# Optimization experiments

Measured on AMD Instinct MI355X. Metric: run time of the kernel, lower is better.

## Reference

```python
import jax, jax.numpy as jnp
import numpy as np

B, IN, HID, OUT, E, C, TOPK = 4096, 1024, 2048, 1024, 8, 1000, 2
EPS = 1e-6


def setup_inputs() -> dict:
    key = jax.random.key(0)
    ks = jax.random.split(key, 8)
    def xavier(k, fan_out, fan_in):
        lim = float(np.sqrt(6.0 / (fan_in + fan_out)))
        return jax.random.uniform(k, (fan_out, fan_in), jnp.float32, -lim, lim)
    return {
        "x": jax.random.normal(ks[0], (B, IN), jnp.float32),
        "Wg": xavier(ks[1], E, IN),
        "bg": jnp.zeros((E,), jnp.float32),
        "gamma": jnp.ones((1, E), jnp.float32),
        "beta": jnp.zeros((1, E), jnp.float32),
        "W1": xavier(ks[2], HID * E, IN),
        "b1": jnp.zeros((HID * E,), jnp.float32),
        "W2": xavier(ks[3], OUT * E, HID * E),
        "b2": jnp.zeros((OUT * E,), jnp.float32),
        "Wc": xavier(ks[4], C, OUT),
        "bc": jnp.zeros((C,), jnp.float32),
    }


def reference(x, Wg, bg, gamma, beta, W1, b1, W2, b2, Wc, bc):
    # gating (noise_std=0 -> no noise)
    gate_logits = x @ Wg.T + bg                      # [B, E]
    # GRN over expert dim
    Gx = jnp.linalg.norm(gate_logits, axis=1, keepdims=True)   # [B, 1]
    Nx = Gx / (jnp.mean(Gx, axis=0, keepdims=True) + EPS)      # [B, 1]
    gate_logits = gamma * (gate_logits * Nx) + beta
    gate_probs = jax.nn.softmax(gate_logits, axis=-1)
    topk_probs, topk_idx = jax.lax.top_k(gate_probs, TOPK)     # [B, K]
    # dense all-expert MLP (fc2 mixes across ALL experts' hidden units, as in source)
    h = jax.nn.relu(x @ W1.T + b1)                   # [B, HID*E]
    eo = (h @ W2.T + b2).reshape(B, E, OUT)          # [B, E, OUT]
    sel = jnp.take_along_axis(eo, topk_idx[:, :, None], axis=1)  # [B, K, OUT]
    out = jnp.einsum('bk,bkd->bd', topk_probs, sel)  # [B, OUT]
    return out @ Wc.T + bc                           # [B, C]
```

## Files before the change

kernel.cpp:

```cpp
#include <hip/hip_runtime.h>
#include <stdint.h>

#define B_SZ   4096
#define IN_SZ  1024
#define NE     8
#define NC     1000
#define HIDE   16384
#define OUTE   1024
#define GEPS   1e-6f

typedef __attribute__((ext_vector_type(8))) short short8;
typedef __attribute__((ext_vector_type(4))) float floatx4;

__device__ __forceinline__ unsigned short f2bf(float f) {
    unsigned u = __float_as_uint(f);
    u += 0x7fffu + ((u >> 16) & 1u);
    return (unsigned short)(u >> 16);
}
__device__ __forceinline__ float bf2f(unsigned short h) {
    return __uint_as_float(((unsigned)h) << 16);
}

__device__ __forceinline__ void async16(const void* g, void* l) {
    __builtin_amdgcn_global_load_lds(
        (const __attribute__((address_space(1))) void*)g,
        (__attribute__((address_space(3))) void*)l, 16, 0, 0);
}

__global__ __launch_bounds__(256) void k_cvt(const float* __restrict__ src,
                                             unsigned short* __restrict__ dst, int n) {
    int i = (blockIdx.x * 256 + threadIdx.x) * 4;
    int stride = gridDim.x * 256 * 4;
    for (; i < n; i += stride) {
        float4 v = *(const float4*)(src + i);
        ushort4 o;
        o.x = f2bf(v.x); o.y = f2bf(v.y); o.z = f2bf(v.z); o.w = f2bf(v.w);
        *(ushort4*)(dst + i) = o;
    }
}

__global__ __launch_bounds__(256) void k_gate(const float* __restrict__ x,
                                              const float* __restrict__ Wg,
                                              const float* __restrict__ bg,
                                              float* __restrict__ logits,
                                              float* __restrict__ Gx) {
    int wid = threadIdx.x >> 6, lane = threadIdx.x & 63;
    int b = blockIdx.x * 4 + wid;
    const float* xr = x + (size_t)b * IN_SZ;
    float xv[16];
#pragma unroll
    for (int t = 0; t < 16; ++t) xv[t] = xr[lane + 64 * t];
    float lg[NE];
#pragma unroll
    for (int e = 0; e < NE; ++e) {
        const float* wr = Wg + e * IN_SZ;
        float s = 0.f;
#pragma unroll
        for (int t = 0; t < 16; ++t) s += xv[t] * wr[lane + 64 * t];
#pragma unroll
        for (int m = 32; m >= 1; m >>= 1) s += __shfl_xor(s, m, 64);
        lg[e] = s + bg[e];
    }
    if (lane == 0) {
        float ss = 0.f;
#pragma unroll
        for (int e = 0; e < NE; ++e) { logits[b * NE + e] = lg[e]; ss += lg[e] * lg[e]; }
        Gx[b] = sqrtf(ss);
    }
}

__global__ __launch_bounds__(1024) void k_gsum(const float* __restrict__ Gx, float* __restrict__ gsum) {
    __shared__ float sm[1024];
    int t = threadIdx.x;
    sm[t] = Gx[t] + Gx[t + 1024] + Gx[t + 2048] + Gx[t + 3072];
    __syncthreads();
    for (int m = 512; m >= 1; m >>= 1) {
        if (t < m) sm[t] += sm[t + m];
        __syncthreads();
    }
    if (t == 0) gsum[0] = sm[0];
}

__global__ void k_zeroctrl(int* ctrl) {
    if (threadIdx.x < 24) ctrl[threadIdx.x] = 0;
}

__global__ __launch_bounds__(256) void k_topk(const float* __restrict__ logits,
                                              const float* __restrict__ Gx,
                                              const float* __restrict__ gsum,
                                              const float* __restrict__ gamma,
                                              const float* __restrict__ beta,
                                              int* __restrict__ tidx, float* __restrict__ tp,
                                              int* __restrict__ counts) {
    int b = blockIdx.x * 256 + threadIdx.x;
    float nx = Gx[b] / (gsum[0] * (1.0f / (float)B_SZ) + GEPS);
    float l[NE];
    float mx = -1e30f;
#pragma unroll
    for (int e = 0; e < NE; ++e) {
        l[e] = gamma[e] * (logits[b * NE + e] * nx) + beta[e];
        mx = fmaxf(mx, l[e]);
    }
    float se = 0.f;
#pragma unroll
    for (int e = 0; e < NE; ++e) { l[e] = expf(l[e] - mx); se += l[e]; }
    float inv = 1.f / se;
    int i0 = 0; float p0 = l[0];
#pragma unroll
    for (int e = 1; e < NE; ++e) if (l[e] > p0) { p0 = l[e]; i0 = e; }
    int i1 = -1; float p1 = -1.f;
#pragma unroll
    for (int e = 0; e < NE; ++e) if (e != i0 && l[e] > p1) { p1 = l[e]; i1 = e; }
    tidx[b * 2 + 0] = i0; tidx[b * 2 + 1] = i1;
    tp[b * 2 + 0] = p0 * inv; tp[b * 2 + 1] = p1 * inv;
    atomicAdd(&counts[i0], 1);
    atomicAdd(&counts[i1], 1);
}

__global__ void k_offsets(const int* __restrict__ counts, int* __restrict__ offs) {
    if (threadIdx.x == 0) {
        int a = 0;
        for (int e = 0; e < NE; ++e) { offs[e] = a; a += counts[e]; }
    }
}

__global__ __launch_bounds__(256) void k_fill(const int* __restrict__ tidx, const float* __restrict__ tp,
                                              const int* __restrict__ offs, int* __restrict__ cursors,
                                              int* __restrict__ rowsw, float* __restrict__ probsw) {
    int b = blockIdx.x * 256 + threadIdx.x;
#pragma unroll
    for (int k = 0; k < 2; ++k) {
        int e = tidx[b * 2 + k];
        int pos = atomicAdd(&cursors[e], 1);
        int at = offs[e] + pos;
        rowsw[at] = b * 2 + k;
        probsw[at] = tp[b * 2 + k];
    }
}

__device__ __forceinline__ void gemm_core(const unsigned short* sa0, const unsigned short* sa1,
                                          const unsigned short* sb0, const unsigned short* sb1,
                                          short* sA, short* sB, int nkt, int wid, int lane,
                                          floatx4 acc[4][4]) {
    short* ldsA0 = sA + (wid * 2 + 0) * 512;
    short* ldsA1 = sA + (wid * 2 + 1) * 512;
    short* ldsB0 = sB + (wid * 2 + 0) * 512;
    short* ldsB1 = sB + (wid * 2 + 1) * 512;
    const int wm = wid >> 1, wn = wid & 1;
    int aoff[4], boff[4];
#pragma unroll
    for (int i = 0; i < 4; ++i) {
        aoff[i] = (wm * 64 + i * 16 + (lane & 15)) * 32 + (lane >> 4) * 8;
        boff[i] = (wn * 64 + i * 16 + (lane & 15)) * 32 + (lane >> 4) * 8;
    }
    for (int kt = 0; kt < nkt; ++kt) {
        __syncthreads();
        async16(sa0, ldsA0);
        async16(sa1, ldsA1);
        async16(sb0, ldsB0);
        async16(sb1, ldsB1);
        sa0 += 32; sa1 += 32; sb0 += 32; sb1 += 32;
        __syncthreads();
        short8 av[4], bv[4];
#pragma unroll
        for (int i = 0; i < 4; ++i) av[i] = *(const short8*)(sA + aoff[i]);
#pragma unroll
        for (int j = 0; j < 4; ++j) bv[j] = *(const short8*)(sB + boff[j]);
#pragma unroll
        for (int i = 0; i < 4; ++i)
#pragma unroll
            for (int j = 0; j < 4; ++j)
                acc[i][j] = __builtin_amdgcn_mfma_f32_16x16x32_bf16(av[i], bv[j], acc[i][j], 0, 0, 0);
    }
}

__global__ __launch_bounds__(256) void k_gemm_h(const unsigned short* __restrict__ xb,
                                                const unsigned short* __restrict__ w1b,
                                                const float* __restrict__ b1,
                                                unsigned short* __restrict__ h) {
    __shared__ __align__(16) short sA[128 * 32];
    __shared__ __align__(16) short sB[128 * 32];
    const int lane = threadIdx.x & 63, wid = threadIdx.x >> 6;
    const int mt = blockIdx.x & 31, nt = blockIdx.x >> 5;
    const int m0 = mt * 128, n0 = nt * 128;
    const int t0row = (wid * 2 + 0) * 16 + (lane >> 2);
    const int t1row = (wid * 2 + 1) * 16 + (lane >> 2);
    const int kb = (lane & 3) * 8;
    const unsigned short* sa0 = xb + (size_t)(m0 + t0row) * IN_SZ + kb;
    const unsigned short* sa1 = xb + (size_t)(m0 + t1row) * IN_SZ + kb;
    const unsigned short* sb0 = w1b + (size_t)(n0 + t0row) * IN_SZ + kb;
    const unsigned short* sb1 = w1b + (size_t)(n0 + t1row) * IN_SZ + kb;
    floatx4 acc[4][4] = {};
    gemm_core(sa0, sa1, sb0, sb1, sA, sB, IN_SZ / 32, wid, lane, acc);
    const int wm = wid >> 1, wn = wid & 1;
#pragma unroll
    for (int i = 0; i < 4; ++i)
#pragma unroll
        for (int j = 0; j < 4; ++j)
#pragma unroll
            for (int r = 0; r < 4; ++r) {
                int row = m0 + wm * 64 + i * 16 + (lane >> 4) * 4 + r;
                int col = n0 + wn * 64 + j * 16 + (lane & 15);
                float v = acc[i][j][r] + b1[col];
                h[(size_t)row * HIDE + col] = f2bf(fmaxf(v, 0.f));
            }
}

__global__ __launch_bounds__(256) void k_gemm_moe(const unsigned short* __restrict__ h,
                                                  const unsigned short* __restrict__ w2b,
                                                  const float* __restrict__ b2,
                                                  const int* __restrict__ counts,
                                                  const int* __restrict__ offs,
                                                  const int* __restrict__ rowsw,
                                                  const float* __restrict__ probsw,
                                                  unsigned short* __restrict__ slotbuf) {
    const int bid = blockIdx.x;
    const int e = bid >> 8;
    const int rem = bid & 255;
    const int mt = rem >> 3, nt = rem & 7;
    const int gn = counts[e];
    if (mt * 128 >= gn) return;
    const int gbase = offs[e];
    __shared__ __align__(16) short sA[128 * 32];
    __shared__ __align__(16) short sB[128 * 32];
    const int lane = threadIdx.x & 63, wid = threadIdx.x >> 6;
    const int t0row = (wid * 2 + 0) * 16 + (lane >> 2);
    const int t1row = (wid * 2 + 1) * 16 + (lane >> 2);
    const int kb = (lane & 3) * 8;
    int g0 = mt * 128 + t0row; if (g0 > gn - 1) g0 = gn - 1;
    int g1 = mt * 128 + t1row; if (g1 > gn - 1) g1 = gn - 1;
    const int rv0 = rowsw[gbase + g0] >> 1;
    const int rv1 = rowsw[gbase + g1] >> 1;
    const int n0 = nt * 128;
    const unsigned short* sa0 = h + (size_t)rv0 * HIDE + kb;
    const unsigned short* sa1 = h + (size_t)rv1 * HIDE + kb;
    const unsigned short* sb0 = w2b + (size_t)(e * OUTE + n0 + t0row) * HIDE + kb;
    const unsigned short* sb1 = w2b + (size_t)(e * OUTE + n0 + t1row) * HIDE + kb;
    floatx4 acc[4][4] = {};
    gemm_core(sa0, sa1, sb0, sb1, sA, sB, HIDE / 32, wid, lane, acc);
    const int wm = wid >> 1, wn = wid & 1;
#pragma unroll
    for (int i = 0; i < 4; ++i)
#pragma unroll
        for (int j = 0; j < 4; ++j)
#pragma unroll
            for (int r = 0; r < 4; ++r) {
                int lr = mt * 128 + wm * 64 + i * 16 + (lane >> 4) * 4 + r;
                if (lr < gn) {
                    int at = gbase + lr;
                    int dest = rowsw[at];
                    float p = probsw[at];
                    int col = n0 + wn * 64 + j * 16 + (lane & 15);
                    float v = (acc[i][j][r] + b2[e * OUTE + col]) * p;
                    slotbuf[(size_t)dest * OUTE + col] = f2bf(v);
                }
            }
}

__global__ __launch_bounds__(256) void k_combine(const unsigned short* __restrict__ slotbuf,
                                                 unsigned short* __restrict__ ymix) {
    int i = blockIdx.x * 256 + threadIdx.x;
    int b = i >> 7;
    int d = (i & 127) * 8;
    short8 s0 = *(const short8*)(slotbuf + (size_t)(b * 2 + 0) * OUTE + d);
    short8 s1 = *(const short8*)(slotbuf + (size_t)(b * 2 + 1) * OUTE + d);
    short8 o;
#pragma unroll
    for (int t = 0; t < 8; ++t)
        o[t] = (short)f2bf(bf2f((unsigned short)s0[t]) + bf2f((unsigned short)s1[t]));
    *(short8*)(ymix + (size_t)b * OUTE + d) = o;
}

__global__ __launch_bounds__(256) void k_gemm_out(const unsigned short* __restrict__ ymix,
                                                  const unsigned short* __restrict__ wcb,
                                                  const float* __restrict__ bc,
                                                  float* __restrict__ out) {
    const int mt = blockIdx.x >> 3, nt = blockIdx.x & 7;
    const int m0 = mt * 128, n0 = nt * 128;
    __shared__ __align__(16) short sA[128 * 32];
    __shared__ __align__(16) short sB[128 * 32];
    const int lane = threadIdx.x & 63, wid = threadIdx.x >> 6;
    const int t0row = (wid * 2 + 0) * 16 + (lane >> 2);
    const int t1row = (wid * 2 + 1) * 16 + (lane >> 2);
    const int kb = (lane & 3) * 8;
    int br0 = n0 + t0row; if (br0 > NC - 1) br0 = NC - 1;
    int br1 = n0 + t1row; if (br1 > NC - 1) br1 = NC - 1;
    const unsigned short* sa0 = ymix + (size_t)(m0 + t0row) * IN_SZ + kb;
    const unsigned short* sa1 = ymix + (size_t)(m0 + t1row) * IN_SZ + kb;
    const unsigned short* sb0 = wcb + (size_t)br0 * IN_SZ + kb;
    const unsigned short* sb1 = wcb + (size_t)br1 * IN_SZ + kb;
    floatx4 acc[4][4] = {};
    gemm_core(sa0, sa1, sb0, sb1, sA, sB, IN_SZ / 32, wid, lane, acc);
    const int wm = wid >> 1, wn = wid & 1;
#pragma unroll
    for (int i = 0; i < 4; ++i)
#pragma unroll
        for (int j = 0; j < 4; ++j)
#pragma unroll
            for (int r = 0; r < 4; ++r) {
                int row = m0 + wm * 64 + i * 16 + (lane >> 4) * 4 + r;
                int col = n0 + wn * 64 + j * 16 + (lane & 15);
                if (col < NC)
                    out[(size_t)row * NC + col] = acc[i][j][r] + bc[col];
            }
}

extern "C" void kernel_launch(void* const* d_in, const int* in_sizes, int n_in,
                              void* d_out, int out_size, void* d_ws, size_t ws_size,
                              hipStream_t stream) {
    const float* x     = (const float*)d_in[0];
    const float* Wg    = (const float*)d_in[1];
    const float* bg    = (const float*)d_in[2];
    const float* gamma = (const float*)d_in[3];
    const float* beta  = (const float*)d_in[4];
    const float* W1    = (const float*)d_in[5];
    const float* b1    = (const float*)d_in[6];
    const float* W2    = (const float*)d_in[7];
    const float* b2    = (const float*)d_in[8];
    const float* Wc    = (const float*)d_in[9];
    const float* bc    = (const float*)d_in[10];
    float* out = (float*)d_out;

    char* ws = (char*)d_ws;
    size_t o = 0;
    auto carve = [&](size_t bytes) { char* p = ws + o; o += (bytes + 255) & ~(size_t)255; return p; };
    unsigned short* xb   = (unsigned short*)carve((size_t)B_SZ * IN_SZ * 2);
    unsigned short* w1b  = (unsigned short*)carve((size_t)HIDE * IN_SZ * 2);
    unsigned short* w2b  = (unsigned short*)carve((size_t)NE * OUTE * HIDE * 2);
    unsigned short* wcb  = (unsigned short*)carve((size_t)NC * IN_SZ * 2);
    unsigned short* h    = (unsigned short*)carve((size_t)B_SZ * HIDE * 2);
    unsigned short* slot = (unsigned short*)carve((size_t)B_SZ * 2 * OUTE * 2);
    unsigned short* ymix = (unsigned short*)carve((size_t)B_SZ * OUTE * 2);
    float* logits = (float*)carve((size_t)B_SZ * NE * 4);
    float* Gx     = (float*)carve((size_t)B_SZ * 4);
    int*   tidx   = (int*)carve((size_t)B_SZ * 2 * 4);
    float* tp     = (float*)carve((size_t)B_SZ * 2 * 4);
    int*   rowsw  = (int*)carve((size_t)B_SZ * 2 * 4);
    float* probsw = (float*)carve((size_t)B_SZ * 2 * 4);
    int*   ctrl   = (int*)carve(256);
    int* counts  = ctrl;
    int* cursors = ctrl + 8;
    int* offs    = ctrl + 16;
    float* gsum  = (float*)(ctrl + 24);

    k_cvt<<<2048, 256, 0, stream>>>(x,  xb,  B_SZ * IN_SZ);
    k_cvt<<<2048, 256, 0, stream>>>(W1, w1b, HIDE * IN_SZ);
    k_cvt<<<2048, 256, 0, stream>>>(W2, w2b, NE * OUTE * HIDE);
    k_cvt<<<2048, 256, 0, stream>>>(Wc, wcb, NC * IN_SZ);

    k_gate<<<B_SZ / 4, 256, 0, stream>>>(x, Wg, bg, logits, Gx);
    k_gsum<<<1, 1024, 0, stream>>>(Gx, gsum);
    k_zeroctrl<<<1, 64, 0, stream>>>(ctrl);
    k_topk<<<B_SZ / 256, 256, 0, stream>>>(logits, Gx, gsum, gamma, beta, tidx, tp, counts);
    k_offsets<<<1, 64, 0, stream>>>(counts, offs);
    k_fill<<<B_SZ / 256, 256, 0, stream>>>(tidx, tp, offs, cursors, rowsw, probsw);

    k_gemm_h<<<32 * (HIDE / 128), 256, 0, stream>>>(xb, w1b, b1, h);
    k_gemm_moe<<<NE * 32 * 8, 256, 0, stream>>>(h, w2b, b2, counts, offs, rowsw, probsw, slot);
    k_combine<<<(B_SZ * OUTE / 8) / 256, 256, 0, stream>>>(slot, ymix);
    k_gemm_out<<<32 * 8, 256, 0, stream>>>(ymix, wcb, bc, out);
}
```

Before: 1.018 ms.

## Replace both big GEMMs with 256x256 double-buffered 8-wave kernels and split-K MoE

The fc1 and per-expert fc2 GEMMs move from 128x128 single-buffered tiles to 256x256 tiles with 512 threads and 128KB of dynamic LDS. The new kernels use XOR-swizzled LDS layouts, double buffering with staged async loads, setprio around MFMA groups, and an XCD-aware block remap. The MoE GEMM is split four ways along K into bf16 partial buffers. A new reduce kernel sums the partials, adds bias and applies the gate-weighted combine, replacing the old epilogue and combine kernel. This aims to raise MFMA utilisation and data reuse, at the cost of extra partial-buffer traffic and bf16 rounding of the partial sums.

Measured after the change: 1.274 ms. 1.25x slower.

```diff
diff --git a/kernel.cpp b/kernel.cpp
--- a/kernel.cpp
+++ b/kernel.cpp
@@ -8,6 +8,10 @@
 #define HIDE   16384
 #define OUTE   1024
 #define GEPS   1e-6f
+#define NSPLIT 4
+#define KSPL   4096
+#define NT_MOE 64
+#define NT_H   16
 
 typedef __attribute__((ext_vector_type(8))) short short8;
 typedef __attribute__((ext_vector_type(4))) float floatx4;
@@ -25,6 +29,12 @@
     __builtin_amdgcn_global_load_lds(
         (const __attribute__((address_space(1))) void*)g,
         (__attribute__((address_space(3))) void*)l, 16, 0, 0);
+}
+
+__device__ __forceinline__ void stage_half(const unsigned short* p0, const unsigned short* p1,
+                                           char* smemc, int ldsoff, int w, int tt) {
+    async16(p0 + (size_t)tt * 64, smemc + ldsoff + w * 1024);
+    async16(p1 + (size_t)tt * 64, smemc + ldsoff + 8192 + w * 1024);
 }
 
 __global__ __launch_bounds__(256) void k_cvt(const float* __restrict__ src,
@@ -126,7 +136,7 @@
 
 __global__ __launch_bounds__(256) void k_fill(const int* __restrict__ tidx, const float* __restrict__ tp,
                                               const int* __restrict__ offs, int* __restrict__ cursors,
-                                              int* __restrict__ rowsw, float* __restrict__ probsw) {
+                                              int* __restrict__ rowsw, int* __restrict__ slotof) {
     int b = blockIdx.x * 256 + threadIdx.x;
 #pragma unroll
     for (int k = 0; k < 2; ++k) {
@@ -134,8 +144,196 @@
         int pos = atomicAdd(&cursors[e], 1);
         int at = offs[e] + pos;
         rowsw[at] = b * 2 + k;
-        probsw[at] = tp[b * 2 + k];
-    }
+        slotof[b * 2 + k] = at;
+    }
+}
+
+
+#define MFMA_PAIR(JA, JB) \
+  __builtin_amdgcn_s_setprio(1); \
+  _Pragma("unroll") \
+  for (int i_ = 0; i_ < 8; ++i_) { \
+    acc[i_][JA] = __builtin_amdgcn_mfma_f32_16x16x32_bf16(av[i_], bva, acc[i_][JA], 0, 0, 0); \
+    acc[i_][JB] = __builtin_amdgcn_mfma_f32_16x16x32_bf16(av[i_], bvb, acc[i_][JB], 0, 0, 0); \
+  } \
+  __builtin_amdgcn_s_setprio(0);
+
+#define BARSYNC  __builtin_amdgcn_s_barrier(); __builtin_amdgcn_sched_barrier(0);
+
+#define TILE_BODY(T_, BUF_, NTT_) do { \
+  const int tq1_ = (T_) + 1, tq2_ = (T_) + 2; \
+  if (tq1_ < (NTT_)) { \
+    stage_half(pA[1][0], pA[1][1], smemc, ((tq1_ & 1) * 65536) + 16384, w, tq1_); \
+    asm volatile("s_waitcnt vmcnt(4)" ::: "memory"); \
+  } else { \
+    asm volatile("s_waitcnt vmcnt(0)" ::: "memory"); \
+  } \
+  BARSYNC \
+  { \
+  const short* Ab_ = smem + (BUF_) * 32768 + wm * 8192; \
+  const short* Bb_ = smem + (BUF_) * 32768 + 16384 + (wn >> 1) * 8192; \
+  short8 av[8], bva, bvb; \
+  _Pragma("unroll") \
+  for (int i_ = 0; i_ < 8; ++i_) av[i_] = *(const short8*)(Ab_ + aoff[i_]); \
+  bva = *(const short8*)(Bb_ + boff[0]); \
+  bvb = *(const short8*)(Bb_ + boff[1]); \
+  MFMA_PAIR(0, 1) \
+  BARSYNC \
+  bva = *(const short8*)(Bb_ + boff[2]); \
+  bvb = *(const short8*)(Bb_ + boff[3]); \
+  if (tq1_ < (NTT_)) stage_half(pB[0][0], pB[0][1], smemc, ((tq1_ & 1) * 65536) + 32768, w, tq1_); \
+  MFMA_PAIR(2, 3) \
+  BARSYNC \
+  _Pragma("unroll") \
+  for (int i_ = 0; i_ < 8; ++i_) av[i_] = *(const short8*)(Ab_ + (aoff[i_] ^ 32)); \
+  bva = *(const short8*)(Bb_ + (boff[0] ^ 32)); \
+  bvb = *(const short8*)(Bb_ + (boff[1] ^ 32)); \
+  if (tq1_ < (NTT_)) stage_half(pB[1][0], pB[1][1], smemc, ((tq1_ & 1) * 65536) + 49152, w, tq1_); \
+  MFMA_PAIR(0, 1) \
+  BARSYNC \
+  bva = *(const short8*)(Bb_ + (boff[2] ^ 32)); \
+  bvb = *(const short8*)(Bb_ + (boff[3] ^ 32)); \
+  if (tq2_ < (NTT_)) stage_half(pA[0][0], pA[0][1], smemc, ((tq2_ & 1) * 65536) + 0, w, tq2_); \
+  MFMA_PAIR(2, 3) \
+  BARSYNC \
+  } \
+} while (0)
+
+#define CORE_PROLOGUE(NTT_) \
+  stage_half(pA[0][0], pA[0][1], smemc, 0,     w, 0); \
+  stage_half(pA[1][0], pA[1][1], smemc, 16384, w, 0); \
+  stage_half(pB[0][0], pB[0][1], smemc, 32768, w, 0); \
+  stage_half(pB[1][0], pB[1][1], smemc, 49152, w, 0); \
+  if ((NTT_) > 1) stage_half(pA[0][0], pA[0][1], smemc, 65536, w, 1);
+
+__global__ __launch_bounds__(512, 1) void k_h8(const unsigned short* __restrict__ xb,
+                                               const unsigned short* __restrict__ w1b,
+                                               const float* __restrict__ b1,
+                                               unsigned short* __restrict__ hout) {
+    extern __shared__ short smem[];
+    char* smemc = (char*)smem;
+    const int tid = threadIdx.x, lane = tid & 63, w = tid >> 6;
+    const int wm = w >> 2, wn = w & 3;
+    const int q = gridDim.x >> 3;
+    const int wg = (blockIdx.x & 7) * q + (blockIdx.x >> 3);
+    const int mt = wg & 15, nt = wg >> 4;
+    const int m0 = mt * 256, n0 = nt * 256;
+    const int ccs = ((lane & 7) ^ (lane >> 3)) * 8;
+    const unsigned short* pA[2][2];
+    const unsigned short* pB[2][2];
+#pragma unroll
+    for (int h = 0; h < 2; ++h)
+#pragma unroll
+        for (int c = 0; c < 2; ++c) {
+            pA[h][c] = xb  + (size_t)(m0 + h * 128 + c * 64 + w * 8 + (lane >> 3)) * IN_SZ + ccs;
+            pB[h][c] = w1b + (size_t)(n0 + h * 128 + c * 64 + w * 8 + (lane >> 3)) * IN_SZ + ccs;
+        }
+    int aoff[8], boff[4];
+#pragma unroll
+    for (int i = 0; i < 8; ++i)
+        aoff[i] = (i * 16 + (lane & 15)) * 64 + (((lane >> 4) ^ (lane & 7)) * 8);
+#pragma unroll
+    for (int j = 0; j < 4; ++j)
+        boff[j] = ((wn & 1) * 64 + j * 16 + (lane & 15)) * 64 + (((lane >> 4) ^ (lane & 7)) * 8);
+    floatx4 acc[8][4] = {};
+    CORE_PROLOGUE(NT_H)
+    for (int t = 0; t < NT_H; t += 2) { TILE_BODY(t, 0, NT_H); TILE_BODY(t + 1, 1, NT_H); }
+#pragma unroll
+    for (int i = 0; i < 8; ++i)
+#pragma unroll
+        for (int j = 0; j < 4; ++j)
+#pragma unroll
+            for (int r = 0; r < 4; ++r) {
+                int row = m0 + wm * 128 + i * 16 + (lane >> 4) * 4 + r;
+                int col = n0 + wn * 64 + j * 16 + (lane & 15);
+                float v = acc[i][j][r] + b1[col];
+                hout[(size_t)row * HIDE + col] = f2bf(fmaxf(v, 0.f));
+            }
+}
+
+__global__ __launch_bounds__(512, 1) void k_moe8(const unsigned short* __restrict__ h,
+                                                 const unsigned short* __restrict__ w2b,
+                                                 const int* __restrict__ counts,
+                                                 const int* __restrict__ offs,
+                                                 const int* __restrict__ rowsw,
+                                                 unsigned short* __restrict__ parts) {
+    extern __shared__ short smem[];
+    char* smemc = (char*)smem;
+    const int q = gridDim.x >> 3;
+    const int wg = (blockIdx.x & 7) * q + (blockIdx.x >> 3);
+    const int mt = wg & 15, sp = (wg >> 4) & 3, nt = (wg >> 6) & 3, e = wg >> 8;
+    const int gn = counts[e];
+    if (mt * 256 >= gn) return;
+    const int gbase = offs[e];
+    const int tid = threadIdx.x, lane = tid & 63, w = tid >> 6;
+    const int wm = w >> 2, wn = w & 3;
+    const int ccs = ((lane & 7) ^ (lane >> 3)) * 8;
+    const unsigned short* pA[2][2];
+    const unsigned short* pB[2][2];
+#pragma unroll
+    for (int hh = 0; hh < 2; ++hh)
+#pragma unroll
+        for (int c = 0; c < 2; ++c) {
+            int lr = mt * 256 + hh * 128 + c * 64 + w * 8 + (lane >> 3);
+            if (lr > gn - 1) lr = gn - 1;
+            int grow = rowsw[gbase + lr] >> 1;
+            pA[hh][c] = h + (size_t)grow * HIDE + sp * KSPL + ccs;
+            int brow = e * OUTE + nt * 256 + hh * 128 + c * 64 + w * 8 + (lane >> 3);
+            pB[hh][c] = w2b + (size_t)brow * HIDE + sp * KSPL + ccs;
+        }
+    int aoff[8], boff[4];
+#pragma unroll
+    for (int i = 0; i < 8; ++i)
+        aoff[i] = (i * 16 + (lane & 15)) * 64 + (((lane >> 4) ^ (lane & 7)) * 8);
+#pragma unroll
+    for (int j = 0; j < 4; ++j)
+        boff[j] = ((wn & 1) * 64 + j * 16 + (lane & 15)) * 64 + (((lane >> 4) ^ (lane & 7)) * 8);
+    floatx4 acc[8][4] = {};
+    CORE_PROLOGUE(NT_MOE)
+    for (int t = 0; t < NT_MOE; t += 2) { TILE_BODY(t, 0, NT_MOE); TILE_BODY(t + 1, 1, NT_MOE); }
+    unsigned short* pbase = parts + (size_t)sp * B_SZ * 2 * OUTE;
+#pragma unroll
+    for (int i = 0; i < 8; ++i)
+#pragma unroll
+        for (int j = 0; j < 4; ++j)
+#pragma unroll
+            for (int r = 0; r < 4; ++r) {
+                int lr = mt * 256 + wm * 128 + i * 16 + (lane >> 4) * 4 + r;
+                if (lr < gn) {
+                    int at = gbase + lr;
+                    int col = nt * 256 + wn * 64 + j * 16 + (lane & 15);
+                    pbase[(size_t)at * OUTE + col] = f2bf(acc[i][j][r]);
+                }
+            }
+}
+
+__global__ __launch_bounds__(256) void k_reduce(const unsigned short* __restrict__ parts,
+                                                const int* __restrict__ slotof,
+                                                const int* __restrict__ tidx,
+                                                const float* __restrict__ tp,
+                                                const float* __restrict__ b2,
+                                                unsigned short* __restrict__ ymix) {
+    int i = blockIdx.x * 256 + threadIdx.x;
+    int b = i >> 8, col = (i & 255) * 4;
+    int at0 = slotof[b * 2], at1 = slotof[b * 2 + 1];
+    int e0 = tidx[b * 2], e1 = tidx[b * 2 + 1];
+    float q0 = tp[b * 2], q1 = tp[b * 2 + 1];
+    float y0[4] = {0.f, 0.f, 0.f, 0.f}, y1[4] = {0.f, 0.f, 0.f, 0.f};
+#pragma unroll
+    for (int sp = 0; sp < NSPLIT; ++sp) {
+        ushort4 u0 = *(const ushort4*)(parts + ((size_t)sp * B_SZ * 2 + at0) * OUTE + col);
+        ushort4 u1 = *(const ushort4*)(parts + ((size_t)sp * B_SZ * 2 + at1) * OUTE + col);
+        y0[0] += bf2f(u0.x); y0[1] += bf2f(u0.y); y0[2] += bf2f(u0.z); y0[3] += bf2f(u0.w);
+        y1[0] += bf2f(u1.x); y1[1] += bf2f(u1.y); y1[2] += bf2f(u1.z); y1[3] += bf2f(u1.w);
+    }
+    float4 bb0 = *(const float4*)(b2 + (size_t)e0 * OUTE + col);
+    float4 bb1 = *(const float4*)(b2 + (size_t)e1 * OUTE + col);
+    ushort4 o;
+    o.x = f2bf(q0 * (y0[0] + bb0.x) + q1 * (y1[0] + bb1.x));
+    o.y = f2bf(q0 * (y0[1] + bb0.y) + q1 * (y1[1] + bb1.y));
+    o.z = f2bf(q0 * (y0[2] + bb0.z) + q1 * (y1[2] + bb1.z));
+    o.w = f2bf(q0 * (y0[3] + bb0.w) + q1 * (y1[3] + bb1.w));
+    *(ushort4*)(ymix + (size_t)b * OUTE + col) = o;
 }
 
 __device__ __forceinline__ void gemm_core(const unsigned short* sa0, const unsigned short* sa1,
@@ -172,103 +370,6 @@
             for (int j = 0; j < 4; ++j)
                 acc[i][j] = __builtin_amdgcn_mfma_f32_16x16x32_bf16(av[i], bv[j], acc[i][j], 0, 0, 0);
     }
-}
-
-__global__ __launch_bounds__(256) void k_gemm_h(const unsigned short* __restrict__ xb,
-                                                const unsigned short* __restrict__ w1b,
-                                                const float* __restrict__ b1,
-                                                unsigned short* __restrict__ h) {
-    __shared__ __align__(16) short sA[128 * 32];
-    __shared__ __align__(16) short sB[128 * 32];
-    const int lane = threadIdx.x & 63, wid = threadIdx.x >> 6;
-    const int mt = blockIdx.x & 31, nt = blockIdx.x >> 5;
-    const int m0 = mt * 128, n0 = nt * 128;
-    const int t0row = (wid * 2 + 0) * 16 + (lane >> 2);
-    const int t1row = (wid * 2 + 1) * 16 + (lane >> 2);
-    const int kb = (lane & 3) * 8;
-    const unsigned short* sa0 = xb + (size_t)(m0 + t0row) * IN_SZ + kb;
-    const unsigned short* sa1 = xb + (size_t)(m0 + t1row) * IN_SZ + kb;
-    const unsigned short* sb0 = w1b + (size_t)(n0 + t0row) * IN_SZ + kb;
-    const unsigned short* sb1 = w1b + (size_t)(n0 + t1row) * IN_SZ + kb;
-    floatx4 acc[4][4] = {};
-    gemm_core(sa0, sa1, sb0, sb1, sA, sB, IN_SZ / 32, wid, lane, acc);
-    const int wm = wid >> 1, wn = wid & 1;
-#pragma unroll
-    for (int i = 0; i < 4; ++i)
-#pragma unroll
-        for (int j = 0; j < 4; ++j)
-#pragma unroll
-            for (int r = 0; r < 4; ++r) {
-                int row = m0 + wm * 64 + i * 16 + (lane >> 4) * 4 + r;
-                int col = n0 + wn * 64 + j * 16 + (lane & 15);
-                float v = acc[i][j][r] + b1[col];
-                h[(size_t)row * HIDE + col] = f2bf(fmaxf(v, 0.f));
-            }
-}
-
-__global__ __launch_bounds__(256) void k_gemm_moe(const unsigned short* __restrict__ h,
-                                                  const unsigned short* __restrict__ w2b,
-                                                  const float* __restrict__ b2,
-                                                  const int* __restrict__ counts,
-                                                  const int* __restrict__ offs,
-                                                  const int* __restrict__ rowsw,
-                                                  const float* __restrict__ probsw,
-                                                  unsigned short* __restrict__ slotbuf) {
-    const int bid = blockIdx.x;
-    const int e = bid >> 8;
-    const int rem = bid & 255;
-    const int mt = rem >> 3, nt = rem & 7;
-    const int gn = counts[e];
-    if (mt * 128 >= gn) return;
-    const int gbase = offs[e];
-    __shared__ __align__(16) short sA[128 * 32];
-    __shared__ __align__(16) short sB[128 * 32];
-    const int lane = threadIdx.x & 63, wid = threadIdx.x >> 6;
-    const int t0row = (wid * 2 + 0) * 16 + (lane >> 2);
-    const int t1row = (wid * 2 + 1) * 16 + (lane >> 2);
-    const int kb = (lane & 3) * 8;
-    int g0 = mt * 128 + t0row; if (g0 > gn - 1) g0 = gn - 1;
-    int g1 = mt * 128 + t1row; if (g1 > gn - 1) g1 = gn - 1;
-    const int rv0 = rowsw[gbase + g0] >> 1;
-    const int rv1 = rowsw[gbase + g1] >> 1;
-    const int n0 = nt * 128;
-    const unsigned short* sa0 = h + (size_t)rv0 * HIDE + kb;
-    const unsigned short* sa1 = h + (size_t)rv1 * HIDE + kb;
-    const unsigned short* sb0 = w2b + (size_t)(e * OUTE + n0 + t0row) * HIDE + kb;
-    const unsigned short* sb1 = w2b + (size_t)(e * OUTE + n0 + t1row) * HIDE + kb;
-    floatx4 acc[4][4] = {};
-    gemm_core(sa0, sa1, sb0, sb1, sA, sB, HIDE / 32, wid, lane, acc);
-    const int wm = wid >> 1, wn = wid & 1;
-#pragma unroll
-    for (int i = 0; i < 4; ++i)
-#pragma unroll
-        for (int j = 0; j < 4; ++j)
-#pragma unroll
-            for (int r = 0; r < 4; ++r) {
-                int lr = mt * 128 + wm * 64 + i * 16 + (lane >> 4) * 4 + r;
-                if (lr < gn) {
-                    int at = gbase + lr;
-                    int dest = rowsw[at];
-                    float p = probsw[at];
-                    int col = n0 + wn * 64 + j * 16 + (lane & 15);
-                    float v = (acc[i][j][r] + b2[e * OUTE + col]) * p;
-                    slotbuf[(size_t)dest * OUTE + col] = f2bf(v);
-                }
-            }
-}
-
-__global__ __launch_bounds__(256) void k_combine(const unsigned short* __restrict__ slotbuf,
-                                                 unsigned short* __restrict__ ymix) {
-    int i = blockIdx.x * 256 + threadIdx.x;
-    int b = i >> 7;
-    int d = (i & 127) * 8;
-    short8 s0 = *(const short8*)(slotbuf + (size_t)(b * 2 + 0) * OUTE + d);
-    short8 s1 = *(const short8*)(slotbuf + (size_t)(b * 2 + 1) * OUTE + d);
-    short8 o;
-#pragma unroll
-    for (int t = 0; t < 8; ++t)
-        o[t] = (short)f2bf(bf2f((unsigned short)s0[t]) + bf2f((unsigned short)s1[t]));
-    *(short8*)(ymix + (size_t)b * OUTE + d) = o;
 }
 
 __global__ __launch_bounds__(256) void k_gemm_out(const unsigned short* __restrict__ ymix,
@@ -324,25 +425,28 @@
     char* ws = (char*)d_ws;
     size_t o = 0;
     auto carve = [&](size_t bytes) { char* p = ws + o; o += (bytes + 255) & ~(size_t)255; return p; };
-    unsigned short* xb   = (unsigned short*)carve((size_t)B_SZ * IN_SZ * 2);
-    unsigned short* w1b  = (unsigned short*)carve((size_t)HIDE * IN_SZ * 2);
-    unsigned short* w2b  = (unsigned short*)carve((size_t)NE * OUTE * HIDE * 2);
-    unsigned short* wcb  = (unsigned short*)carve((size_t)NC * IN_SZ * 2);
-    unsigned short* h    = (unsigned short*)carve((size_t)B_SZ * HIDE * 2);
-    unsigned short* slot = (unsigned short*)carve((size_t)B_SZ * 2 * OUTE * 2);
-    unsigned short* ymix = (unsigned short*)carve((size_t)B_SZ * OUTE * 2);
+    unsigned short* xb    = (unsigned short*)carve((size_t)B_SZ * IN_SZ * 2);
+    unsigned short* w1b   = (unsigned short*)carve((size_t)HIDE * IN_SZ * 2);
+    unsigned short* w2b   = (unsigned short*)carve((size_t)NE * OUTE * HIDE * 2);
+    unsigned short* wcb   = (unsigned short*)carve((size_t)NC * IN_SZ * 2);
+    unsigned short* h     = (unsigned short*)carve((size_t)B_SZ * HIDE * 2);
+    unsigned short* parts = (unsigned short*)carve((size_t)NSPLIT * B_SZ * 2 * OUTE * 2);
+    unsigned short* ymix  = (unsigned short*)carve((size_t)B_SZ * OUTE * 2);
     float* logits = (float*)carve((size_t)B_SZ * NE * 4);
     float* Gx     = (float*)carve((size_t)B_SZ * 4);
     int*   tidx   = (int*)carve((size_t)B_SZ * 2 * 4);
     float* tp     = (float*)carve((size_t)B_SZ * 2 * 4);
     int*   rowsw  = (int*)carve((size_t)B_SZ * 2 * 4);
-    float* probsw = (float*)carve((size_t)B_SZ * 2 * 4);
+    int*   slotof = (int*)carve((size_t)B_SZ * 2 * 4);
     int*   ctrl   = (int*)carve(256);
     int* counts  = ctrl;
     int* cursors = ctrl + 8;
     int* offs    = ctrl + 16;
     float* gsum  = (float*)(ctrl + 24);
 
+    hipFuncSetAttribute((const void*)k_h8,   hipFuncAttributeMaxDynamicSharedMemorySize, 131072);
+    hipFuncSetAttribute((const void*)k_moe8, hipFuncAttributeMaxDynamicSharedMemorySize, 131072);
+
     k_cvt<<<2048, 256, 0, stream>>>(x,  xb,  B_SZ * IN_SZ);
     k_cvt<<<2048, 256, 0, stream>>>(W1, w1b, HIDE * IN_SZ);
     k_cvt<<<2048, 256, 0, stream>>>(W2, w2b, NE * OUTE * HIDE);
@@ -353,10 +457,10 @@
     k_zeroctrl<<<1, 64, 0, stream>>>(ctrl);
     k_topk<<<B_SZ / 256, 256, 0, stream>>>(logits, Gx, gsum, gamma, beta, tidx, tp, counts);
     k_offsets<<<1, 64, 0, stream>>>(counts, offs);
-    k_fill<<<B_SZ / 256, 256, 0, stream>>>(tidx, tp, offs, cursors, rowsw, probsw);
-
-    k_gemm_h<<<32 * (HIDE / 128), 256, 0, stream>>>(xb, w1b, b1, h);
-    k_gemm_moe<<<NE * 32 * 8, 256, 0, stream>>>(h, w2b, b2, counts, offs, rowsw, probsw, slot);
-    k_combine<<<(B_SZ * OUTE / 8) / 256, 256, 0, stream>>>(slot, ymix);
-    k_gemm_out<<<32 * 8, 256, 0, stream>>>(ymix, wcb, bc, out);
-}
+    k_fill<<<B_SZ / 256, 256, 0, stream>>>(tidx, tp, offs, cursors, rowsw, slotof);
+
+    k_h8<<<(B_SZ / 256) * (HIDE / 256), 512, 131072, stream>>>(xb, w1b, b1, h);
+    k_moe8<<<NE * 16 * 4 * NSPLIT, 512, 131072, stream>>>(h, w2b, counts, offs, rowsw, parts);
+    k_reduce<<<B_SZ, 256, 0, stream>>>(parts, slotof, tidx, tp, b2, ymix);
+    k_gemm_out<<<(B_SZ / 128) * 8, 256, 0, stream>>>(ymix, wcb, bc, out);
+}
```

## Rework GEMMs with BK=64 swizzled LDS, split-K MoE GEMM, and fused reduce

Applied to the files above, without the earlier changes.

Replaces the hidden-layer and expert GEMMs with a new core that loads 64-wide K tiles into XOR-swizzled LDS, which halves the number of barrier pairs per unit of K and avoids LDS bank conflicts. Workgroup IDs are remapped across the 8 XCDs. The expert GEMM is split along K into two halves to create more workgroups, and the halves write bf16 partial results. A new reduce kernel sums the partials, adds the bias, applies the gate probabilities and combines the two experts, replacing the old combine kernel. The trade-off is extra partial-buffer traffic and a loss of precision from storing partials in bf16.

After: 1.063 ms. 4.5% more time.

```diff
diff --git a/kernel.cpp b/kernel.cpp
--- a/kernel.cpp
+++ b/kernel.cpp
@@ -8,6 +8,8 @@
 #define HIDE   16384
 #define OUTE   1024
 #define GEPS   1e-6f
+#define NSPLIT 2
+#define KSPL   8192
 
 typedef __attribute__((ext_vector_type(8))) short short8;
 typedef __attribute__((ext_vector_type(4))) float floatx4;
@@ -126,7 +128,7 @@
 
 __global__ __launch_bounds__(256) void k_fill(const int* __restrict__ tidx, const float* __restrict__ tp,
                                               const int* __restrict__ offs, int* __restrict__ cursors,
-                                              int* __restrict__ rowsw, float* __restrict__ probsw) {
+                                              int* __restrict__ rowsw, int* __restrict__ slotof) {
     int b = blockIdx.x * 256 + threadIdx.x;
 #pragma unroll
     for (int k = 0; k < 2; ++k) {
@@ -134,8 +136,168 @@
         int pos = atomicAdd(&cursors[e], 1);
         int at = offs[e] + pos;
         rowsw[at] = b * 2 + k;
-        probsw[at] = tp[b * 2 + k];
-    }
+        slotof[b * 2 + k] = at;
+    }
+}
+
+
+__device__ __forceinline__ void core64(
+    const unsigned short* pa0, const unsigned short* pa1,
+    const unsigned short* pa2, const unsigned short* pa3,
+    const unsigned short* pb0, const unsigned short* pb1,
+    const unsigned short* pb2, const unsigned short* pb3,
+    short* sA, short* sB, int nkt, int wm, int wn, int tid, int lane,
+    floatx4 acc[4][4])
+{
+    char* sAc = (char*)sA;
+    char* sBc = (char*)sB;
+    const int sl = ((lane >> 4) ^ (lane & 7)) * 8;
+    int aoff[4], boff[4];
+#pragma unroll
+    for (int i = 0; i < 4; ++i) {
+        aoff[i] = (wm * 64 + i * 16 + (lane & 15)) * 64 + sl;
+        boff[i] = (wn * 64 + i * 16 + (lane & 15)) * 64 + sl;
+    }
+    for (int kt = 0; kt < nkt; ++kt) {
+        __syncthreads();
+        async16(pa0, sAc + tid * 16);
+        async16(pa1, sAc + 4096 + tid * 16);
+        async16(pa2, sAc + 8192 + tid * 16);
+        async16(pa3, sAc + 12288 + tid * 16);
+        async16(pb0, sBc + tid * 16);
+        async16(pb1, sBc + 4096 + tid * 16);
+        async16(pb2, sBc + 8192 + tid * 16);
+        async16(pb3, sBc + 12288 + tid * 16);
+        pa0 += 64; pa1 += 64; pa2 += 64; pa3 += 64;
+        pb0 += 64; pb1 += 64; pb2 += 64; pb3 += 64;
+        __syncthreads();
+        short8 a0[4], a1[4], b0[4], b1[4];
+#pragma unroll
+        for (int i = 0; i < 4; ++i) {
+            a0[i] = *(const short8*)(sA + aoff[i]);
+            a1[i] = *(const short8*)(sA + (aoff[i] ^ 32));
+            b0[i] = *(const short8*)(sB + boff[i]);
+            b1[i] = *(const short8*)(sB + (boff[i] ^ 32));
+        }
+#pragma unroll
+        for (int i = 0; i < 4; ++i)
+#pragma unroll
+            for (int j = 0; j < 4; ++j) {
+                acc[i][j] = __builtin_amdgcn_mfma_f32_16x16x32_bf16(a0[i], b0[j], acc[i][j], 0, 0, 0);
+                acc[i][j] = __builtin_amdgcn_mfma_f32_16x16x32_bf16(a1[i], b1[j], acc[i][j], 0, 0, 0);
+            }
+    }
+}
+
+__global__ __launch_bounds__(256) void k_h8(const unsigned short* __restrict__ xb,
+                                            const unsigned short* __restrict__ w1b,
+                                            const float* __restrict__ b1,
+                                            unsigned short* __restrict__ hout) {
+    __shared__ __align__(16) short sA[128 * 64];
+    __shared__ __align__(16) short sB[128 * 64];
+    const int tid = threadIdx.x, lane = tid & 63, wid = tid >> 6;
+    const int wm = wid >> 1, wn = wid & 1;
+    const int wg = (blockIdx.x & 7) * (gridDim.x >> 3) + (blockIdx.x >> 3);
+    const int mt = wg & 31, nt = wg >> 5;
+    const int m0 = mt * 128, n0 = nt * 128;
+    const int srow = tid >> 3;
+    const int cswz = ((tid & 7) ^ (srow & 7)) * 8;
+    const unsigned short* pa[4];
+    const unsigned short* pb[4];
+#pragma unroll
+    for (int c = 0; c < 4; ++c) {
+        pa[c] = xb  + (size_t)(m0 + 32 * c + srow) * IN_SZ + cswz;
+        pb[c] = w1b + (size_t)(n0 + 32 * c + srow) * IN_SZ + cswz;
+    }
+    floatx4 acc[4][4] = {};
+    core64(pa[0], pa[1], pa[2], pa[3], pb[0], pb[1], pb[2], pb[3],
+           sA, sB, IN_SZ / 64, wm, wn, tid, lane, acc);
+#pragma unroll
+    for (int i = 0; i < 4; ++i)
+#pragma unroll
+        for (int j = 0; j < 4; ++j)
+#pragma unroll
+            for (int r = 0; r < 4; ++r) {
+                int row = m0 + wm * 64 + i * 16 + (lane >> 4) * 4 + r;
+                int col = n0 + wn * 64 + j * 16 + (lane & 15);
+                float v = acc[i][j][r] + b1[col];
+                hout[(size_t)row * HIDE + col] = f2bf(fmaxf(v, 0.f));
+            }
+}
+
+__global__ __launch_bounds__(256) void k_moe(const unsigned short* __restrict__ h,
+                                             const unsigned short* __restrict__ w2b,
+                                             const int* __restrict__ counts,
+                                             const int* __restrict__ offs,
+                                             const int* __restrict__ rowsw,
+                                             unsigned short* __restrict__ parts) {
+    const int wg = (blockIdx.x & 7) * (gridDim.x >> 3) + (blockIdx.x >> 3);
+    const int mt = wg & 31, nt = (wg >> 5) & 7, sp = (wg >> 8) & 1, e = wg >> 9;
+    const int gn = counts[e];
+    if (mt * 128 >= gn) return;
+    const int gbase = offs[e];
+    __shared__ __align__(16) short sA[128 * 64];
+    __shared__ __align__(16) short sB[128 * 64];
+    const int tid = threadIdx.x, lane = tid & 63, wid = tid >> 6;
+    const int wm = wid >> 1, wn = wid & 1;
+    const int srow = tid >> 3;
+    const int cswz = ((tid & 7) ^ (srow & 7)) * 8;
+    const unsigned short* pa[4];
+    const unsigned short* pb[4];
+#pragma unroll
+    for (int c = 0; c < 4; ++c) {
+        int lr = mt * 128 + 32 * c + srow;
+        if (lr > gn - 1) lr = gn - 1;
+        int grow = rowsw[gbase + lr] >> 1;
+        pa[c] = h + (size_t)grow * HIDE + sp * KSPL + cswz;
+        pb[c] = w2b + (size_t)(e * OUTE + nt * 128 + 32 * c + srow) * HIDE + sp * KSPL + cswz;
+    }
+    floatx4 acc[4][4] = {};
+    core64(pa[0], pa[1], pa[2], pa[3], pb[0], pb[1], pb[2], pb[3],
+           sA, sB, KSPL / 64, wm, wn, tid, lane, acc);
+    unsigned short* pbase = parts + (size_t)sp * B_SZ * 2 * OUTE;
+#pragma unroll
+    for (int i = 0; i < 4; ++i)
+#pragma unroll
+        for (int j = 0; j < 4; ++j)
+#pragma unroll
+            for (int r = 0; r < 4; ++r) {
+                int lr = mt * 128 + wm * 64 + i * 16 + (lane >> 4) * 4 + r;
+                if (lr < gn) {
+                    int at = gbase + lr;
+                    int col = nt * 128 + wn * 64 + j * 16 + (lane & 15);
+                    pbase[(size_t)at * OUTE + col] = f2bf(acc[i][j][r]);
+                }
+            }
+}
+
+__global__ __launch_bounds__(256) void k_reduce(const unsigned short* __restrict__ parts,
+                                                const int* __restrict__ slotof,
+                                                const int* __restrict__ tidx,
+                                                const float* __restrict__ tp,
+                                                const float* __restrict__ b2,
+                                                unsigned short* __restrict__ ymix) {
+    int i = blockIdx.x * 256 + threadIdx.x;
+    int b = i >> 8, col = (i & 255) * 4;
+    int at0 = slotof[b * 2], at1 = slotof[b * 2 + 1];
+    int e0 = tidx[b * 2], e1 = tidx[b * 2 + 1];
+    float q0 = tp[b * 2], q1 = tp[b * 2 + 1];
+    float y0[4] = {0.f, 0.f, 0.f, 0.f}, y1[4] = {0.f, 0.f, 0.f, 0.f};
+#pragma unroll
+    for (int sp = 0; sp < NSPLIT; ++sp) {
+        ushort4 u0 = *(const ushort4*)(parts + ((size_t)sp * B_SZ * 2 + at0) * OUTE + col);
+        ushort4 u1 = *(const ushort4*)(parts + ((size_t)sp * B_SZ * 2 + at1) * OUTE + col);
+        y0[0] += bf2f(u0.x); y0[1] += bf2f(u0.y); y0[2] += bf2f(u0.z); y0[3] += bf2f(u0.w);
+        y1[0] += bf2f(u1.x); y1[1] += bf2f(u1.y); y1[2] += bf2f(u1.z); y1[3] += bf2f(u1.w);
+    }
+    float4 bb0 = *(const float4*)(b2 + (size_t)e0 * OUTE + col);
+    float4 bb1 = *(const float4*)(b2 + (size_t)e1 * OUTE + col);
+    ushort4 o;
+    o.x = f2bf(q0 * (y0[0] + bb0.x) + q1 * (y1[0] + bb1.x));
+    o.y = f2bf(q0 * (y0[1] + bb0.y) + q1 * (y1[1] + bb1.y));
+    o.z = f2bf(q0 * (y0[2] + bb0.z) + q1 * (y1[2] + bb1.z));
+    o.w = f2bf(q0 * (y0[3] + bb0.w) + q1 * (y1[3] + bb1.w));
+    *(ushort4*)(ymix + (size_t)b * OUTE + col) = o;
 }
 
 __device__ __forceinline__ void gemm_core(const unsigned short* sa0, const unsigned short* sa1,
@@ -172,103 +334,6 @@
             for (int j = 0; j < 4; ++j)
                 acc[i][j] = __builtin_amdgcn_mfma_f32_16x16x32_bf16(av[i], bv[j], acc[i][j], 0, 0, 0);
     }
-}
-
-__global__ __launch_bounds__(256) void k_gemm_h(const unsigned short* __restrict__ xb,
-                                                const unsigned short* __restrict__ w1b,
-                                                const float* __restrict__ b1,
-                                                unsigned short* __restrict__ h) {
-    __shared__ __align__(16) short sA[128 * 32];
-    __shared__ __align__(16) short sB[128 * 32];
-    const int lane = threadIdx.x & 63, wid = threadIdx.x >> 6;
-    const int mt = blockIdx.x & 31, nt = blockIdx.x >> 5;
-    const int m0 = mt * 128, n0 = nt * 128;
-    const int t0row = (wid * 2 + 0) * 16 + (lane >> 2);
-    const int t1row = (wid * 2 + 1) * 16 + (lane >> 2);
-    const int kb = (lane & 3) * 8;
-    const unsigned short* sa0 = xb + (size_t)(m0 + t0row) * IN_SZ + kb;
-    const unsigned short* sa1 = xb + (size_t)(m0 + t1row) * IN_SZ + kb;
-    const unsigned short* sb0 = w1b + (size_t)(n0 + t0row) * IN_SZ + kb;
-    const unsigned short* sb1 = w1b + (size_t)(n0 + t1row) * IN_SZ + kb;
-    floatx4 acc[4][4] = {};
-    gemm_core(sa0, sa1, sb0, sb1, sA, sB, IN_SZ / 32, wid, lane, acc);
-    const int wm = wid >> 1, wn = wid & 1;
-#pragma unroll
-    for (int i = 0; i < 4; ++i)
-#pragma unroll
-        for (int j = 0; j < 4; ++j)
-#pragma unroll
-            for (int r = 0; r < 4; ++r) {
-                int row = m0 + wm * 64 + i * 16 + (lane >> 4) * 4 + r;
-                int col = n0 + wn * 64 + j * 16 + (lane & 15);
-                float v = acc[i][j][r] + b1[col];
-                h[(size_t)row * HIDE + col] = f2bf(fmaxf(v, 0.f));
-            }
-}
-
-__global__ __launch_bounds__(256) void k_gemm_moe(const unsigned short* __restrict__ h,
-                                                  const unsigned short* __restrict__ w2b,
-                                                  const float* __restrict__ b2,
-                                                  const int* __restrict__ counts,
-                                                  const int* __restrict__ offs,
-                                                  const int* __restrict__ rowsw,
-                                                  const float* __restrict__ probsw,
-                                                  unsigned short* __restrict__ slotbuf) {
-    const int bid = blockIdx.x;
-    const int e = bid >> 8;
-    const int rem = bid & 255;
-    const int mt = rem >> 3, nt = rem & 7;
-    const int gn = counts[e];
-    if (mt * 128 >= gn) return;
-    const int gbase = offs[e];
-    __shared__ __align__(16) short sA[128 * 32];
-    __shared__ __align__(16) short sB[128 * 32];
-    const int lane = threadIdx.x & 63, wid = threadIdx.x >> 6;
-    const int t0row = (wid * 2 + 0) * 16 + (lane >> 2);
-    const int t1row = (wid * 2 + 1) * 16 + (lane >> 2);
-    const int kb = (lane & 3) * 8;
-    int g0 = mt * 128 + t0row; if (g0 > gn - 1) g0 = gn - 1;
-    int g1 = mt * 128 + t1row; if (g1 > gn - 1) g1 = gn - 1;
-    const int rv0 = rowsw[gbase + g0] >> 1;
-    const int rv1 = rowsw[gbase + g1] >> 1;
-    const int n0 = nt * 128;
-    const unsigned short* sa0 = h + (size_t)rv0 * HIDE + kb;
-    const unsigned short* sa1 = h + (size_t)rv1 * HIDE + kb;
-    const unsigned short* sb0 = w2b + (size_t)(e * OUTE + n0 + t0row) * HIDE + kb;
-    const unsigned short* sb1 = w2b + (size_t)(e * OUTE + n0 + t1row) * HIDE + kb;
-    floatx4 acc[4][4] = {};
-    gemm_core(sa0, sa1, sb0, sb1, sA, sB, HIDE / 32, wid, lane, acc);
-    const int wm = wid >> 1, wn = wid & 1;
-#pragma unroll
-    for (int i = 0; i < 4; ++i)
-#pragma unroll
-        for (int j = 0; j < 4; ++j)
-#pragma unroll
-            for (int r = 0; r < 4; ++r) {
-                int lr = mt * 128 + wm * 64 + i * 16 + (lane >> 4) * 4 + r;
-                if (lr < gn) {
-                    int at = gbase + lr;
-                    int dest = rowsw[at];
-                    float p = probsw[at];
-                    int col = n0 + wn * 64 + j * 16 + (lane & 15);
-                    float v = (acc[i][j][r] + b2[e * OUTE + col]) * p;
-                    slotbuf[(size_t)dest * OUTE + col] = f2bf(v);
-                }
-            }
-}
-
-__global__ __launch_bounds__(256) void k_combine(const unsigned short* __restrict__ slotbuf,
-                                                 unsigned short* __restrict__ ymix) {
-    int i = blockIdx.x * 256 + threadIdx.x;
-    int b = i >> 7;
-    int d = (i & 127) * 8;
-    short8 s0 = *(const short8*)(slotbuf + (size_t)(b * 2 + 0) * OUTE + d);
-    short8 s1 = *(const short8*)(slotbuf + (size_t)(b * 2 + 1) * OUTE + d);
-    short8 o;
-#pragma unroll
-    for (int t = 0; t < 8; ++t)
-        o[t] = (short)f2bf(bf2f((unsigned short)s0[t]) + bf2f((unsigned short)s1[t]));
-    *(short8*)(ymix + (size_t)b * OUTE + d) = o;
 }
 
 __global__ __launch_bounds__(256) void k_gemm_out(const unsigned short* __restrict__ ymix,
@@ -324,19 +389,19 @@
     char* ws = (char*)d_ws;
     size_t o = 0;
     auto carve = [&](size_t bytes) { char* p = ws + o; o += (bytes + 255) & ~(size_t)255; return p; };
-    unsigned short* xb   = (unsigned short*)carve((size_t)B_SZ * IN_SZ * 2);
-    unsigned short* w1b  = (unsigned short*)carve((size_t)HIDE * IN_SZ * 2);
-    unsigned short* w2b  = (unsigned short*)carve((size_t)NE * OUTE * HIDE * 2);
-    unsigned short* wcb  = (unsigned short*)carve((size_t)NC * IN_SZ * 2);
-    unsigned short* h    = (unsigned short*)carve((size_t)B_SZ * HIDE * 2);
-    unsigned short* slot = (unsigned short*)carve((size_t)B_SZ * 2 * OUTE * 2);
-    unsigned short* ymix = (unsigned short*)carve((size_t)B_SZ * OUTE * 2);
+    unsigned short* xb    = (unsigned short*)carve((size_t)B_SZ * IN_SZ * 2);
+    unsigned short* w1b   = (unsigned short*)carve((size_t)HIDE * IN_SZ * 2);
+    unsigned short* w2b   = (unsigned short*)carve((size_t)NE * OUTE * HIDE * 2);
+    unsigned short* wcb   = (unsigned short*)carve((size_t)NC * IN_SZ * 2);
+    unsigned short* h     = (unsigned short*)carve((size_t)B_SZ * HIDE * 2);
+    unsigned short* parts = (unsigned short*)carve((size_t)NSPLIT * B_SZ * 2 * OUTE * 2);
+    unsigned short* ymix  = (unsigned short*)carve((size_t)B_SZ * OUTE * 2);
     float* logits = (float*)carve((size_t)B_SZ * NE * 4);
     float* Gx     = (float*)carve((size_t)B_SZ * 4);
     int*   tidx   = (int*)carve((size_t)B_SZ * 2 * 4);
     float* tp     = (float*)carve((size_t)B_SZ * 2 * 4);
     int*   rowsw  = (int*)carve((size_t)B_SZ * 2 * 4);
-    float* probsw = (float*)carve((size_t)B_SZ * 2 * 4);
+    int*   slotof = (int*)carve((size_t)B_SZ * 2 * 4);
     int*   ctrl   = (int*)carve(256);
     int* counts  = ctrl;
     int* cursors = ctrl + 8;
@@ -353,10 +418,10 @@
     k_zeroctrl<<<1, 64, 0, stream>>>(ctrl);
     k_topk<<<B_SZ / 256, 256, 0, stream>>>(logits, Gx, gsum, gamma, beta, tidx, tp, counts);
     k_offsets<<<1, 64, 0, stream>>>(counts, offs);
-    k_fill<<<B_SZ / 256, 256, 0, stream>>>(tidx, tp, offs, cursors, rowsw, probsw);
-
-    k_gemm_h<<<32 * (HIDE / 128), 256, 0, stream>>>(xb, w1b, b1, h);
-    k_gemm_moe<<<NE * 32 * 8, 256, 0, stream>>>(h, w2b, b2, counts, offs, rowsw, probsw, slot);
-    k_combine<<<(B_SZ * OUTE / 8) / 256, 256, 0, stream>>>(slot, ymix);
-    k_gemm_out<<<32 * 8, 256, 0, stream>>>(ymix, wcb, bc, out);
-}
+    k_fill<<<B_SZ / 256, 256, 0, stream>>>(tidx, tp, offs, cursors, rowsw, slotof);
+
+    k_h8<<<(B_SZ / 128) * (HIDE / 128), 256, 0, stream>>>(xb, w1b, b1, h);
+    k_moe<<<NE * 32 * 8 * NSPLIT, 256, 0, stream>>>(h, w2b, counts, offs, rowsw, parts);
+    k_reduce<<<B_SZ, 256, 0, stream>>>(parts, slotof, tidx, tp, b2, ymix);
+    k_gemm_out<<<(B_SZ / 128) * 8, 256, 0, stream>>>(ymix, wcb, bc, out);
+}
```
